# Kernel optimization log

Measured on AMD Instinct MI355X. Metric: run time of the kernel, lower is better.

## Reference

```python
import jax, jax.numpy as jnp
import numpy as np

IN_DIM = 512
OUT_DIM = 256


def setup_inputs() -> dict:
    key = jax.random.key(0)
    ks = jax.random.split(key, 5)
    b, n, d, o = 32, 64, IN_DIM, OUT_DIM
    lim1 = 1.0 / np.sqrt(2 * d)
    lim2 = 1.0 / np.sqrt(o)
    return {
        "x": jax.random.normal(ks[0], (b, n, d), dtype=jnp.float32),
        "W1": jax.random.uniform(ks[1], (o, 2 * d), jnp.float32, -lim1, lim1),
        "b1": jax.random.uniform(ks[2], (o,), jnp.float32, -lim1, lim1),
        "W2": jax.random.uniform(ks[3], (o, o), jnp.float32, -lim2, lim2),
        "b2": jax.random.uniform(ks[4], (o,), jnp.float32, -lim2, lim2),
    }


def reference(x, W1, b1, W2, b2):
    # x: [b, n, d]; fc1 over cat(xi, xj) == xi @ Wa.T + xj @ Wb.T + b1
    b, n, d = x.shape
    Wa, Wb = W1[:, :d], W1[:, d:]
    hi = jnp.einsum("bnd,od->bno", x, Wa)  # [b, n, o]
    hj = jnp.einsum("bnd,od->bno", x, Wb)  # [b, n, o]
    h = hi[:, :, None, :] + hj[:, None, :, :] + b1  # [b, n, n, o]
    y = jax.nn.relu(jnp.einsum("bijo,po->bijp", h, W2) + b2)  # [b, n, n, o]
    mask = ~jnp.eye(n, dtype=bool)  # zero self-pairs
    y = y * mask[None, :, :, None]
    return y.sum(axis=2)  # [b, n, o]
```

## Files before the change

### kernel.cpp

```cpp
#include <hip/hip_runtime.h>
#include <hip/hip_bf16.h>


typedef unsigned short u16;
typedef __attribute__((ext_vector_type(8))) short short8v;
typedef __attribute__((ext_vector_type(4))) short short4v;
typedef __attribute__((ext_vector_type(4))) float float4v;

typedef __attribute__((address_space(1))) const unsigned char* gas_ptr;
typedef __attribute__((address_space(3))) unsigned char* las_ptr;

__device__ __forceinline__ void lds_load16(const void* g, void* l) {
    __builtin_amdgcn_global_load_lds((gas_ptr)g, (las_ptr)l, 16, 0, 0);
}

__device__ __forceinline__ u16 f2bf(float f) {
    unsigned u = __float_as_uint(f);
    return (u16)((u + 0x7fffu + ((u >> 16) & 1u)) >> 16);
}

__device__ __forceinline__ short8v cvt8v(float4v a, float4v b) {
    union { u16 us[8]; short8v v; } o;
    o.us[0] = f2bf(a.x); o.us[1] = f2bf(a.y); o.us[2] = f2bf(a.z); o.us[3] = f2bf(a.w);
    o.us[4] = f2bf(b.x); o.us[5] = f2bf(b.y); o.us[6] = f2bf(b.z); o.us[7] = f2bf(b.w);
    return o.v;
}

__global__ __launch_bounds__(256) void prep_kernel(
    const float* __restrict__ W1, const float* __restrict__ b1,
    const float* __restrict__ W2, const float* __restrict__ b2,
    u16* __restrict__ Wfb, float* __restrict__ cvec) {
    const int bid = blockIdx.x;
    const int t = threadIdx.x;
    if (bid == 64) {
        float acc = b2[t];
        const float4v* wrow = (const float4v*)(W2 + t * 256);
#pragma unroll 8
        for (int o4 = 0; o4 < 64; ++o4) {
            float4v wv = wrow[o4];
            float4v bv = *(const float4v*)(b1 + o4 * 4);
            acc += wv.x * bv.x + wv.y * bv.y + wv.z * bv.z + wv.w * bv.w;
        }
        cvec[t] = acc;
        return;
    }

    __shared__ __align__(16) u16 As[64 * 264];
    __shared__ __align__(16) u16 Bt[64 * 264];
    const int qt = bid >> 3, dt = bid & 7;
    const int q0 = qt * 64, d0 = dt * 64;
    const int p0 = q0 & 255;
    const int off = (q0 & 256) * 2;
    const int lane = t & 63, w = t >> 6;

#pragma unroll
    for (int rr = 0; rr < 8; ++rr) {
        int row = w * 16 + rr * 2 + (lane >> 5);
        int c = lane & 31;
        const float* s = W2 + (p0 + row) * 256 + c * 8;
        float4v a0 = *(const float4v*)s, a1 = *(const float4v*)(s + 4);
        *(short8v*)&As[row * 264 + c * 8] = cvt8v(a0, a1);
    }
#pragma unroll
    for (int kk = 0; kk < 4; ++kk) {
        const int m = t & 15, og = t >> 4;
        const int o0 = kk * 64 + og * 4;
        const int d4 = m * 4;
        float4v f0 = *(const float4v*)(W1 + (o0 + 0) * 1024 + off + d0 + d4);
        float4v f1 = *(const float4v*)(W1 + (o0 + 1) * 1024 + off + d0 + d4);
        float4v f2 = *(const float4v*)(W1 + (o0 + 2) * 1024 + off + d0 + d4);
        float4v f3 = *(const float4v*)(W1 + (o0 + 3) * 1024 + off + d0 + d4);
        const int u = o0 >> 3, sub = o0 & 7;
#pragma unroll
        for (int dd = 0; dd < 4; ++dd) {
            int d = d4 + dd;
            int usw = u ^ ((d >> 3) & 7);
            union { u16 us[4]; short4v v; } pk;
            pk.us[0] = f2bf(f0[dd]); pk.us[1] = f2bf(f1[dd]);
            pk.us[2] = f2bf(f2[dd]); pk.us[3] = f2bf(f3[dd]);
            *(short4v*)&Bt[d * 264 + usw * 8 + sub] = pk.v;
        }
    }
    __syncthreads();

    const int wm = w >> 1, wn = w & 1;
    const int rQ = lane >> 4, rM = lane & 15;
    float4v acc[2][2] = {};
#pragma unroll
    for (int ks = 0; ks < 8; ++ks) {
        short8v a[2], bf[2];
#pragma unroll
        for (int mf = 0; mf < 2; ++mf) {
            int row = wm * 32 + mf * 16 + rM;
            a[mf] = *(const short8v*)&As[row * 264 + (ks * 4 + rQ) * 8];
        }
#pragma unroll
        for (int nf = 0; nf < 2; ++nf) {
            int drow = wn * 32 + nf * 16 + rM;
            int ku = (ks * 4 + rQ) ^ ((drow >> 3) & 7);
            bf[nf] = *(const short8v*)&Bt[drow * 264 + ku * 8];
        }
#pragma unroll
        for (int mf = 0; mf < 2; ++mf)
#pragma unroll
            for (int nf = 0; nf < 2; ++nf)
                acc[mf][nf] = __builtin_amdgcn_mfma_f32_16x16x32_bf16(
                    a[mf], bf[nf], acc[mf][nf], 0, 0, 0);
    }

#pragma unroll
    for (int mf = 0; mf < 2; ++mf)
#pragma unroll
        for (int nf = 0; nf < 2; ++nf)
#pragma unroll
            for (int r = 0; r < 4; ++r) {
                int q = q0 + wm * 32 + mf * 16 + rQ * 4 + r;
                int d = d0 + wn * 32 + nf * 16 + rM;
                Wfb[q * 512 + d] = f2bf(acc[mf][nf][r]);
            }
}

__global__ __launch_bounds__(512) void fused_kernel(
    const float* __restrict__ x, const u16* __restrict__ Wfb,
    const float* __restrict__ cvec, float* __restrict__ out) {
    __shared__ __align__(16) u16 smem[2 * 64 * 520];
    u16* Xs = smem;
    u16* Ws = smem + 64 * 520;
    const int bid = blockIdx.x;
    const int b = bid & 31, pc = bid >> 5;
    const int p0 = pc * 32;
    const int tid = threadIdx.x;
    const int lane = tid & 63, w = tid >> 6;

#pragma unroll
    for (int rr = 0; rr < 8; ++rr) {
        int row = w * 8 + rr;
        int q = (row < 32) ? (p0 + row) : (256 + p0 + (row - 32));
        lds_load16(Wfb + q * 512 + lane * 8, (void*)&Ws[row * 520]);
    }
#pragma unroll
    for (int rr = 0; rr < 8; ++rr) {
        int row = w * 8 + rr;
        const float* s = x + (b * 64 + row) * 512 + lane * 8;
        float4v a0 = *(const float4v*)s, a1 = *(const float4v*)(s + 4);
        *(short8v*)&Xs[row * 520 + lane * 8] = cvt8v(a0, a1);
    }
    __syncthreads();

    const int uv = w & 1, rh = w >> 1;
    const int rQ = lane >> 4, rM = lane & 15;
    float4v acc[2] = {};
#pragma unroll
    for (int ks = 0; ks < 16; ++ks) {
        int arow = rh * 16 + rM;
        short8v a = *(const short8v*)&Xs[arow * 520 + (ks * 4 + rQ) * 8];
#pragma unroll
        for (int nf = 0; nf < 2; ++nf) {
            int brow = uv * 32 + nf * 16 + rM;
            short8v bf = *(const short8v*)&Ws[brow * 520 + (ks * 4 + rQ) * 8];
            acc[nf] = __builtin_amdgcn_mfma_f32_16x16x32_bf16(a, bf, acc[nf], 0, 0, 0);
        }
    }
    __syncthreads();

    float* Us = (float*)smem;
    float* Vs = Us + 64 * 33;
    float* dst = uv ? Vs : Us;
#pragma unroll
    for (int nf = 0; nf < 2; ++nf)
#pragma unroll
        for (int r = 0; r < 4; ++r)
            dst[(rh * 16 + rQ * 4 + r) * 33 + nf * 16 + rM] = acc[nf][r];
    __syncthreads();

    const int p = tid & 31;
    const int g = tid >> 5;
    const float cv = cvec[p0 + p];
    float uf[4], red[4];
#pragma unroll
    for (int ii = 0; ii < 4; ++ii) {
        uf[ii] = Us[(g * 4 + ii) * 33 + p] + cv;
        red[ii] = 0.f;
    }
#pragma unroll 8
    for (int j = 0; j < 64; ++j) {
        float vs = Vs[j * 33 + p];
#pragma unroll
        for (int ii = 0; ii < 4; ++ii)
            red[ii] += fmaxf(uf[ii] + vs, 0.f);
    }
#pragma unroll
    for (int ii = 0; ii < 4; ++ii) {
        int i = g * 4 + ii;
        red[ii] -= fmaxf(uf[ii] + Vs[i * 33 + p], 0.f);
        out[(b * 64 + i) * 256 + p0 + p] = red[ii];
    }
}

extern "C" void kernel_launch(void* const* d_in, const int* in_sizes, int n_in,
                              void* d_out, int out_size, void* d_ws, size_t ws_size,
                              hipStream_t stream) {
    const float* x  = (const float*)d_in[0];
    const float* W1 = (const float*)d_in[1];
    const float* b1 = (const float*)d_in[2];
    const float* W2 = (const float*)d_in[3];
    const float* b2 = (const float*)d_in[4];
    float* out = (float*)d_out;

    u16* Wfb = (u16*)d_ws;
    float* cvec = (float*)(Wfb + 512 * 512);

    prep_kernel<<<65, 256, 0, stream>>>(W1, b1, W2, b2, Wfb, cvec);
    fused_kernel<<<256, 512, 0, stream>>>(x, Wfb, cvec, out);
}
```

Measured before the change: 21.36 us.

## Merge prep and fused kernels into one launch with a grid-wide atomic barrier

Folds the weight-folding prep kernel into the main kernel. The first 65 blocks compute Wfb and cvec, then every block waits on a global atomic counter before loading Wfb. The x load and bf16 conversion are moved ahead of the barrier so they overlap with the prep work. The pairwise ReLU-sum stage is changed to use 256 threads, each handling two output columns with float2 loads and a padded LDS stride. The aim is to remove one kernel launch and the gap between the two kernels. In exchange it adds a memset, a spin-wait that relies on all 256 blocks being co-resident, and an LDS footprint of about 134KB per block.

After: 46.53 us. 2.18x slower.

```diff
diff --git a/kernel.cpp b/kernel.cpp
--- a/kernel.cpp
+++ b/kernel.cpp
@@ -6,6 +6,7 @@
 typedef __attribute__((ext_vector_type(8))) short short8v;
 typedef __attribute__((ext_vector_type(4))) short short4v;
 typedef __attribute__((ext_vector_type(4))) float float4v;
+typedef __attribute__((ext_vector_type(2))) float float2v;
 
 typedef __attribute__((address_space(1))) const unsigned char* gas_ptr;
 typedef __attribute__((address_space(3))) unsigned char* las_ptr;
@@ -26,111 +27,113 @@
     return o.v;
 }
 
-__global__ __launch_bounds__(256) void prep_kernel(
-    const float* __restrict__ W1, const float* __restrict__ b1,
-    const float* __restrict__ W2, const float* __restrict__ b2,
-    u16* __restrict__ Wfb, float* __restrict__ cvec) {
+#define LDS_TOTAL (66560 + 67584)
+
+__global__ __launch_bounds__(512, 1) void mono_kernel(
+    const float* __restrict__ x, const float* __restrict__ W1,
+    const float* __restrict__ b1, const float* __restrict__ W2,
+    const float* __restrict__ b2,
+    u16* __restrict__ Wfb, float* __restrict__ cvec,
+    unsigned* __restrict__ ctr, float* __restrict__ out) {
+    __shared__ __align__(16) unsigned char smem[LDS_TOTAL];
+    u16* Xs = (u16*)smem;
+    u16* As = (u16*)(smem + 66560);
+    u16* Bt = (u16*)(smem + 66560 + 33792);
+    u16* Ws = (u16*)(smem + 66560);
+
     const int bid = blockIdx.x;
-    const int t = threadIdx.x;
-    if (bid == 64) {
-        float acc = b2[t];
-        const float4v* wrow = (const float4v*)(W2 + t * 256);
+    const int tid = threadIdx.x;
+    const int lane = tid & 63, w = tid >> 6;
+    const int b = ((bid & 7) << 2) | ((bid >> 3) & 3);
+    const int pc = bid >> 5;
+    const int p0 = pc * 32;
+    const int rQ = lane >> 4, rM = lane & 15;
+
+#pragma unroll
+    for (int rr = 0; rr < 8; ++rr) {
+        int row = w * 8 + rr;
+        const float* s = x + (b * 64 + row) * 512 + lane * 8;
+        float4v a0 = *(const float4v*)s, a1 = *(const float4v*)(s + 4);
+        *(short8v*)&Xs[row * 520 + lane * 8] = cvt8v(a0, a1);
+    }
+
+    if (bid < 64) {
+        const int q0 = (bid >> 3) * 64;
+        const int d0 = (bid & 7) * 64;
+        const int pw = q0 & 255;
+        const int off = (q0 & 256) * 2;
+
+#pragma unroll
+        for (int rr = 0; rr < 4; ++rr) {
+            int row = w * 8 + rr * 2 + (lane >> 5);
+            int c = lane & 31;
+            const float* s = W2 + (pw + row) * 256 + c * 8;
+            float4v a0 = *(const float4v*)s, a1 = *(const float4v*)(s + 4);
+            *(short8v*)&As[row * 264 + c * 8] = cvt8v(a0, a1);
+        }
+#pragma unroll
+        for (int kk = 0; kk < 2; ++kk) {
+            const int m = tid & 15, og = tid >> 4;
+            const int o0 = kk * 128 + og * 4;
+            const int d4 = m * 4;
+            float4v f0 = *(const float4v*)(W1 + (o0 + 0) * 1024 + off + d0 + d4);
+            float4v f1 = *(const float4v*)(W1 + (o0 + 1) * 1024 + off + d0 + d4);
+            float4v f2 = *(const float4v*)(W1 + (o0 + 2) * 1024 + off + d0 + d4);
+            float4v f3 = *(const float4v*)(W1 + (o0 + 3) * 1024 + off + d0 + d4);
+            const int u = o0 >> 3, sub = o0 & 7;
+#pragma unroll
+            for (int dd = 0; dd < 4; ++dd) {
+                int d = d4 + dd;
+                int usw = u ^ ((d >> 3) & 7);
+                union { u16 us[4]; short4v v; } pk;
+                pk.us[0] = f2bf(f0[dd]); pk.us[1] = f2bf(f1[dd]);
+                pk.us[2] = f2bf(f2[dd]); pk.us[3] = f2bf(f3[dd]);
+                *(short4v*)&Bt[d * 264 + usw * 8 + sub] = pk.v;
+            }
+        }
+        __syncthreads();
+
+        const int wm = w >> 1, wn = w & 1;
+        float4v pacc[2] = {};
+#pragma unroll
+        for (int ks = 0; ks < 8; ++ks) {
+            short8v a = *(const short8v*)&As[(wm * 16 + rM) * 264 + (ks * 4 + rQ) * 8];
+#pragma unroll
+            for (int nf = 0; nf < 2; ++nf) {
+                int drow = wn * 32 + nf * 16 + rM;
+                int ku = (ks * 4 + rQ) ^ ((drow >> 3) & 7);
+                short8v bf = *(const short8v*)&Bt[drow * 264 + ku * 8];
+                pacc[nf] = __builtin_amdgcn_mfma_f32_16x16x32_bf16(a, bf, pacc[nf], 0, 0, 0);
+            }
+        }
+#pragma unroll
+        for (int nf = 0; nf < 2; ++nf)
+#pragma unroll
+            for (int r = 0; r < 4; ++r) {
+                int q = q0 + wm * 16 + rQ * 4 + r;
+                int d = d0 + wn * 32 + nf * 16 + rM;
+                Wfb[q * 512 + d] = f2bf(pacc[nf][r]);
+            }
+    } else if (bid == 64 && tid < 256) {
+        float acc = b2[tid];
+        const float4v* wrow = (const float4v*)(W2 + tid * 256);
 #pragma unroll 8
         for (int o4 = 0; o4 < 64; ++o4) {
             float4v wv = wrow[o4];
             float4v bv = *(const float4v*)(b1 + o4 * 4);
             acc += wv.x * bv.x + wv.y * bv.y + wv.z * bv.z + wv.w * bv.w;
         }
-        cvec[t] = acc;
-        return;
-    }
-
-    __shared__ __align__(16) u16 As[64 * 264];
-    __shared__ __align__(16) u16 Bt[64 * 264];
-    const int qt = bid >> 3, dt = bid & 7;
-    const int q0 = qt * 64, d0 = dt * 64;
-    const int p0 = q0 & 255;
-    const int off = (q0 & 256) * 2;
-    const int lane = t & 63, w = t >> 6;
-
-#pragma unroll
-    for (int rr = 0; rr < 8; ++rr) {
-        int row = w * 16 + rr * 2 + (lane >> 5);
-        int c = lane & 31;
-        const float* s = W2 + (p0 + row) * 256 + c * 8;
-        float4v a0 = *(const float4v*)s, a1 = *(const float4v*)(s + 4);
-        *(short8v*)&As[row * 264 + c * 8] = cvt8v(a0, a1);
-    }
-#pragma unroll
-    for (int kk = 0; kk < 4; ++kk) {
-        const int m = t & 15, og = t >> 4;
-        const int o0 = kk * 64 + og * 4;
-        const int d4 = m * 4;
-        float4v f0 = *(const float4v*)(W1 + (o0 + 0) * 1024 + off + d0 + d4);
-        float4v f1 = *(const float4v*)(W1 + (o0 + 1) * 1024 + off + d0 + d4);
-        float4v f2 = *(const float4v*)(W1 + (o0 + 2) * 1024 + off + d0 + d4);
-        float4v f3 = *(const float4v*)(W1 + (o0 + 3) * 1024 + off + d0 + d4);
-        const int u = o0 >> 3, sub = o0 & 7;
-#pragma unroll
-        for (int dd = 0; dd < 4; ++dd) {
-            int d = d4 + dd;
-            int usw = u ^ ((d >> 3) & 7);
-            union { u16 us[4]; short4v v; } pk;
-            pk.us[0] = f2bf(f0[dd]); pk.us[1] = f2bf(f1[dd]);
-            pk.us[2] = f2bf(f2[dd]); pk.us[3] = f2bf(f3[dd]);
-            *(short4v*)&Bt[d * 264 + usw * 8 + sub] = pk.v;
-        }
-    }
-    __syncthreads();
-
-    const int wm = w >> 1, wn = w & 1;
-    const int rQ = lane >> 4, rM = lane & 15;
-    float4v acc[2][2] = {};
-#pragma unroll
-    for (int ks = 0; ks < 8; ++ks) {
-        short8v a[2], bf[2];
-#pragma unroll
-        for (int mf = 0; mf < 2; ++mf) {
-            int row = wm * 32 + mf * 16 + rM;
-            a[mf] = *(const short8v*)&As[row * 264 + (ks * 4 + rQ) * 8];
-        }
-#pragma unroll
-        for (int nf = 0; nf < 2; ++nf) {
-            int drow = wn * 32 + nf * 16 + rM;
-            int ku = (ks * 4 + rQ) ^ ((drow >> 3) & 7);
-            bf[nf] = *(const short8v*)&Bt[drow * 264 + ku * 8];
-        }
-#pragma unroll
-        for (int mf = 0; mf < 2; ++mf)
-#pragma unroll
-            for (int nf = 0; nf < 2; ++nf)
-                acc[mf][nf] = __builtin_amdgcn_mfma_f32_16x16x32_bf16(
-                    a[mf], bf[nf], acc[mf][nf], 0, 0, 0);
-    }
-
-#pragma unroll
-    for (int mf = 0; mf < 2; ++mf)
-#pragma unroll
-        for (int nf = 0; nf < 2; ++nf)
-#pragma unroll
-            for (int r = 0; r < 4; ++r) {
-                int q = q0 + wm * 32 + mf * 16 + rQ * 4 + r;
-                int d = d0 + wn * 32 + nf * 16 + rM;
-                Wfb[q * 512 + d] = f2bf(acc[mf][nf][r]);
-            }
-}
-
-__global__ __launch_bounds__(512) void fused_kernel(
-    const float* __restrict__ x, const u16* __restrict__ Wfb,
-    const float* __restrict__ cvec, float* __restrict__ out) {
-    __shared__ __align__(16) u16 smem[2 * 64 * 520];
-    u16* Xs = smem;
-    u16* Ws = smem + 64 * 520;
-    const int bid = blockIdx.x;
-    const int b = bid & 31, pc = bid >> 5;
-    const int p0 = pc * 32;
-    const int tid = threadIdx.x;
-    const int lane = tid & 63, w = tid >> 6;
+        cvec[tid] = acc;
+    }
+
+    __syncthreads();
+    if (tid == 0) {
+        if (bid <= 64)
+            __hip_atomic_fetch_add(ctr, 1u, __ATOMIC_RELEASE, __HIP_MEMORY_SCOPE_AGENT);
+        while (__hip_atomic_load(ctr, __ATOMIC_ACQUIRE, __HIP_MEMORY_SCOPE_AGENT) < 65u)
+            __builtin_amdgcn_s_sleep(4);
+    }
+    __syncthreads();
 
 #pragma unroll
     for (int rr = 0; rr < 8; ++rr) {
@@ -138,22 +141,13 @@
         int q = (row < 32) ? (p0 + row) : (256 + p0 + (row - 32));
         lds_load16(Wfb + q * 512 + lane * 8, (void*)&Ws[row * 520]);
     }
-#pragma unroll
-    for (int rr = 0; rr < 8; ++rr) {
-        int row = w * 8 + rr;
-        const float* s = x + (b * 64 + row) * 512 + lane * 8;
-        float4v a0 = *(const float4v*)s, a1 = *(const float4v*)(s + 4);
-        *(short8v*)&Xs[row * 520 + lane * 8] = cvt8v(a0, a1);
-    }
     __syncthreads();
 
     const int uv = w & 1, rh = w >> 1;
-    const int rQ = lane >> 4, rM = lane & 15;
     float4v acc[2] = {};
 #pragma unroll
     for (int ks = 0; ks < 16; ++ks) {
-        int arow = rh * 16 + rM;
-        short8v a = *(const short8v*)&Xs[arow * 520 + (ks * 4 + rQ) * 8];
+        short8v a = *(const short8v*)&Xs[(rh * 16 + rM) * 520 + (ks * 4 + rQ) * 8];
 #pragma unroll
         for (int nf = 0; nf < 2; ++nf) {
             int brow = uv * 32 + nf * 16 + rM;
@@ -164,36 +158,44 @@
     __syncthreads();
 
     float* Us = (float*)smem;
-    float* Vs = Us + 64 * 33;
+    float* Vs = Us + 64 * 34;
     float* dst = uv ? Vs : Us;
 #pragma unroll
     for (int nf = 0; nf < 2; ++nf)
 #pragma unroll
         for (int r = 0; r < 4; ++r)
-            dst[(rh * 16 + rQ * 4 + r) * 33 + nf * 16 + rM] = acc[nf][r];
-    __syncthreads();
-
-    const int p = tid & 31;
-    const int g = tid >> 5;
-    const float cv = cvec[p0 + p];
-    float uf[4], red[4];
-#pragma unroll
-    for (int ii = 0; ii < 4; ++ii) {
-        uf[ii] = Us[(g * 4 + ii) * 33 + p] + cv;
-        red[ii] = 0.f;
-    }
+            dst[(rh * 16 + rQ * 4 + r) * 34 + nf * 16 + rM] = acc[nf][r];
+    __syncthreads();
+
+    if (tid < 256) {
+        const int p2 = tid & 15;
+        const int ig = tid >> 4;
+        float2v cv = *(const float2v*)(cvec + p0 + p2 * 2);
+        float2v u2[4], acc2[4];
+#pragma unroll
+        for (int ii = 0; ii < 4; ++ii) {
+            float2v uu = *(const float2v*)&Us[(ig * 4 + ii) * 34 + p2 * 2];
+            u2[ii].x = uu.x + cv.x; u2[ii].y = uu.y + cv.y;
+            acc2[ii].x = 0.f; acc2[ii].y = 0.f;
+        }
 #pragma unroll 8
-    for (int j = 0; j < 64; ++j) {
-        float vs = Vs[j * 33 + p];
-#pragma unroll
-        for (int ii = 0; ii < 4; ++ii)
-            red[ii] += fmaxf(uf[ii] + vs, 0.f);
-    }
-#pragma unroll
-    for (int ii = 0; ii < 4; ++ii) {
-        int i = g * 4 + ii;
-        red[ii] -= fmaxf(uf[ii] + Vs[i * 33 + p], 0.f);
-        out[(b * 64 + i) * 256 + p0 + p] = red[ii];
+        for (int j = 0; j < 64; ++j) {
+            float2v v = *(const float2v*)&Vs[j * 34 + p2 * 2];
+#pragma unroll
+            for (int ii = 0; ii < 4; ++ii) {
+                float sx = fmaxf(u2[ii].x + v.x, 0.f);
+                float sy = fmaxf(u2[ii].y + v.y, 0.f);
+                acc2[ii].x += sx; acc2[ii].y += sy;
+            }
+        }
+#pragma unroll
+        for (int ii = 0; ii < 4; ++ii) {
+            int i = ig * 4 + ii;
+            float2v vd = *(const float2v*)&Vs[i * 34 + p2 * 2];
+            acc2[ii].x -= fmaxf(u2[ii].x + vd.x, 0.f);
+            acc2[ii].y -= fmaxf(u2[ii].y + vd.y, 0.f);
+            *(float2v*)&out[(b * 64 + i) * 256 + p0 + p2 * 2] = acc2[ii];
+        }
     }
 }
 
@@ -209,7 +211,8 @@
 
     u16* Wfb = (u16*)d_ws;
     float* cvec = (float*)(Wfb + 512 * 512);
-
-    prep_kernel<<<65, 256, 0, stream>>>(W1, b1, W2, b2, Wfb, cvec);
-    fused_kernel<<<256, 512, 0, stream>>>(x, Wfb, cvec, out);
-}
+    unsigned* ctr = (unsigned*)(cvec + 256);
+
+    hipMemsetAsync(ctr, 0, sizeof(unsigned), stream);
+    mono_kernel<<<256, 512, 0, stream>>>(x, W1, b1, W2, b2, Wfb, cvec, ctr, out);
+}
```

## Pre-convert x to bf16 in prep kernel and load via async LDS in fused kernel

Applied to the files above, without the earlier changes.

Moves the fp32-to-bf16 conversion of x out of the fused kernel into extra blocks of the prep kernel, writing a bf16 copy to workspace. The fused kernel then loads x with global_load_lds, cutting the fp32 read traffic that was repeated across the 8 column blocks per batch. It also vectorises the relu-sum epilogue to float2 with a padded stride of 34 and sets launch bounds to one block per CU. The cost is an extra write and read of the bf16 x buffer and more blocks in the prep launch.

Result: no change. 21.18 us (-0.9%).

```diff
diff --git a/kernel.cpp b/kernel.cpp
--- a/kernel.cpp
+++ b/kernel.cpp
@@ -6,6 +6,7 @@
 typedef __attribute__((ext_vector_type(8))) short short8v;
 typedef __attribute__((ext_vector_type(4))) short short4v;
 typedef __attribute__((ext_vector_type(4))) float float4v;
+typedef __attribute__((ext_vector_type(2))) float float2v;
 
 typedef __attribute__((address_space(1))) const unsigned char* gas_ptr;
 typedef __attribute__((address_space(3))) unsigned char* las_ptr;
@@ -27,11 +28,21 @@
 }
 
 __global__ __launch_bounds__(256) void prep_kernel(
-    const float* __restrict__ W1, const float* __restrict__ b1,
-    const float* __restrict__ W2, const float* __restrict__ b2,
-    u16* __restrict__ Wfb, float* __restrict__ cvec) {
+    const float* __restrict__ x, const float* __restrict__ W1,
+    const float* __restrict__ b1, const float* __restrict__ W2,
+    const float* __restrict__ b2,
+    u16* __restrict__ Wfb, u16* __restrict__ xb, float* __restrict__ cvec) {
     const int bid = blockIdx.x;
     const int t = threadIdx.x;
+    if (bid >= 65) {
+        int base = (bid - 65) * 4096 + t * 16;
+        const float* s = x + base;
+        float4v a0 = *(const float4v*)s,        a1 = *(const float4v*)(s + 4);
+        float4v a2 = *(const float4v*)(s + 8),  a3 = *(const float4v*)(s + 12);
+        *(short8v*)&xb[base]     = cvt8v(a0, a1);
+        *(short8v*)&xb[base + 8] = cvt8v(a2, a3);
+        return;
+    }
     if (bid == 64) {
         float acc = b2[t];
         const float4v* wrow = (const float4v*)(W2 + t * 256);
@@ -52,6 +63,7 @@
     const int p0 = q0 & 255;
     const int off = (q0 & 256) * 2;
     const int lane = t & 63, w = t >> 6;
+    const int rQ = lane >> 4, rM = lane & 15;
 
 #pragma unroll
     for (int rr = 0; rr < 8; ++rr) {
@@ -84,7 +96,6 @@
     __syncthreads();
 
     const int wm = w >> 1, wn = w & 1;
-    const int rQ = lane >> 4, rM = lane & 15;
     float4v acc[2][2] = {};
 #pragma unroll
     for (int ks = 0; ks < 8; ++ks) {
@@ -120,8 +131,8 @@
             }
 }
 
-__global__ __launch_bounds__(512) void fused_kernel(
-    const float* __restrict__ x, const u16* __restrict__ Wfb,
+__global__ __launch_bounds__(512, 1) void fused_kernel(
+    const u16* __restrict__ xb, const u16* __restrict__ Wfb,
     const float* __restrict__ cvec, float* __restrict__ out) {
     __shared__ __align__(16) u16 smem[2 * 64 * 520];
     u16* Xs = smem;
@@ -131,29 +142,26 @@
     const int p0 = pc * 32;
     const int tid = threadIdx.x;
     const int lane = tid & 63, w = tid >> 6;
-
+    const int rQ = lane >> 4, rM = lane & 15;
+    const int uv = w & 1, rh = w >> 1;
+
+#pragma unroll
+    for (int rr = 0; rr < 8; ++rr) {
+        int row = w * 8 + rr;
+        lds_load16(xb + (b * 64 + row) * 512 + lane * 8, (void*)&Xs[row * 520]);
+    }
 #pragma unroll
     for (int rr = 0; rr < 8; ++rr) {
         int row = w * 8 + rr;
         int q = (row < 32) ? (p0 + row) : (256 + p0 + (row - 32));
         lds_load16(Wfb + q * 512 + lane * 8, (void*)&Ws[row * 520]);
     }
-#pragma unroll
-    for (int rr = 0; rr < 8; ++rr) {
-        int row = w * 8 + rr;
-        const float* s = x + (b * 64 + row) * 512 + lane * 8;
-        float4v a0 = *(const float4v*)s, a1 = *(const float4v*)(s + 4);
-        *(short8v*)&Xs[row * 520 + lane * 8] = cvt8v(a0, a1);
-    }
-    __syncthreads();
-
-    const int uv = w & 1, rh = w >> 1;
-    const int rQ = lane >> 4, rM = lane & 15;
+    __syncthreads();
+
     float4v acc[2] = {};
 #pragma unroll
     for (int ks = 0; ks < 16; ++ks) {
-        int arow = rh * 16 + rM;
-        short8v a = *(const short8v*)&Xs[arow * 520 + (ks * 4 + rQ) * 8];
+        short8v a = *(const short8v*)&Xs[(rh * 16 + rM) * 520 + (ks * 4 + rQ) * 8];
 #pragma unroll
         for (int nf = 0; nf < 2; ++nf) {
             int brow = uv * 32 + nf * 16 + rM;
@@ -164,36 +172,41 @@
     __syncthreads();
 
     float* Us = (float*)smem;
-    float* Vs = Us + 64 * 33;
+    float* Vs = Us + 64 * 34;
     float* dst = uv ? Vs : Us;
 #pragma unroll
     for (int nf = 0; nf < 2; ++nf)
 #pragma unroll
         for (int r = 0; r < 4; ++r)
-            dst[(rh * 16 + rQ * 4 + r) * 33 + nf * 16 + rM] = acc[nf][r];
-    __syncthreads();
-
-    const int p = tid & 31;
-    const int g = tid >> 5;
-    const float cv = cvec[p0 + p];
-    float uf[4], red[4];
-#pragma unroll
-    for (int ii = 0; ii < 4; ++ii) {
-        uf[ii] = Us[(g * 4 + ii) * 33 + p] + cv;
-        red[ii] = 0.f;
+            dst[(rh * 16 + rQ * 4 + r) * 34 + nf * 16 + rM] = acc[nf][r];
+    __syncthreads();
+
+    const int p2 = tid & 15;
+    const int ig = tid >> 4;
+    float2v cv = *(const float2v*)(cvec + p0 + p2 * 2);
+    float2v u2[2], acc2[2];
+#pragma unroll
+    for (int ii = 0; ii < 2; ++ii) {
+        float2v uu = *(const float2v*)&Us[(ig * 2 + ii) * 34 + p2 * 2];
+        u2[ii].x = uu.x + cv.x; u2[ii].y = uu.y + cv.y;
+        acc2[ii].x = 0.f; acc2[ii].y = 0.f;
     }
 #pragma unroll 8
     for (int j = 0; j < 64; ++j) {
-        float vs = Vs[j * 33 + p];
-#pragma unroll
-        for (int ii = 0; ii < 4; ++ii)
-            red[ii] += fmaxf(uf[ii] + vs, 0.f);
-    }
-#pragma unroll
-    for (int ii = 0; ii < 4; ++ii) {
-        int i = g * 4 + ii;
-        red[ii] -= fmaxf(uf[ii] + Vs[i * 33 + p], 0.f);
-        out[(b * 64 + i) * 256 + p0 + p] = red[ii];
+        float2v v = *(const float2v*)&Vs[j * 34 + p2 * 2];
+#pragma unroll
+        for (int ii = 0; ii < 2; ++ii) {
+            acc2[ii].x += fmaxf(u2[ii].x + v.x, 0.f);
+            acc2[ii].y += fmaxf(u2[ii].y + v.y, 0.f);
+        }
+    }
+#pragma unroll
+    for (int ii = 0; ii < 2; ++ii) {
+        int i = ig * 2 + ii;
+        float2v vd = *(const float2v*)&Vs[i * 34 + p2 * 2];
+        acc2[ii].x -= fmaxf(u2[ii].x + vd.x, 0.f);
+        acc2[ii].y -= fmaxf(u2[ii].y + vd.y, 0.f);
+        *(float2v*)&out[(b * 64 + i) * 256 + p0 + p2 * 2] = acc2[ii];
     }
 }
 
@@ -208,8 +221,9 @@
     float* out = (float*)d_out;
 
     u16* Wfb = (u16*)d_ws;
-    float* cvec = (float*)(Wfb + 512 * 512);
-
-    prep_kernel<<<65, 256, 0, stream>>>(W1, b1, W2, b2, Wfb, cvec);
-    fused_kernel<<<256, 512, 0, stream>>>(x, Wfb, cvec, out);
-}
+    u16* xb  = Wfb + 512 * 512;
+    float* cvec = (float*)(xb + 2048 * 512);
+
+    prep_kernel<<<321, 256, 0, stream>>>(x, W1, b1, W2, b2, Wfb, xb, cvec);
+    fused_kernel<<<256, 512, 0, stream>>>(xb, Wfb, cvec, out);
+}
```
